# Performance work log

Measured on AMD Instinct MI355X. Metric: run time of the kernel, lower is better.

The kernel has to match this reference:

```python
import jax, jax.numpy as jnp
import numpy as np

EPS = 1e-5  # BatchNorm1d default eps


def gcn_conv(x, src, dst, w, b, n):
    # src/dst already include self-loops. Symmetric normalization D^-1/2 (A+I) D^-1/2.
    deg = jnp.zeros((n,), x.dtype).at[dst].add(1.0)
    dinv = jnp.where(deg > 0, jax.lax.rsqrt(jnp.maximum(deg, 1.0)), 0.0)
    norm = dinv[src] * dinv[dst]                      # [E+N]
    h = x @ w                                          # [B, N, H]
    msg = h[:, src, :] * norm[None, :, None]           # gather + scale  [B, E+N, H]
    agg = jnp.zeros_like(h).at[:, dst, :].add(msg)     # scatter-add
    return agg + b


def batch_norm(h, gamma, beta):
    # training-mode BN over the flattened (B*N) axis, biased variance (torch BN forward)
    mu = h.mean(axis=(0, 1))
    var = ((h - mu) ** 2).mean(axis=(0, 1))
    return (h - mu) * jax.lax.rsqrt(var + EPS) * gamma + beta


def reference(x, edge_index, W1, b1, W2, b2, gamma1, beta1, gamma2, beta2, Wc, bc):
    n = x.shape[1]
    loops = jnp.arange(n)
    src = jnp.concatenate([edge_index[0], loops])
    dst = jnp.concatenate([edge_index[1], loops])
    h = jax.nn.relu(gcn_conv(x, src, dst, W1, b1, n))
    h = batch_norm(h, gamma1, beta1)
    # dropout(p=0.2) treated as identity (eval / deterministic reference)
    h = jax.nn.relu(gcn_conv(h, src, dst, W2, b2, n))
    h = batch_norm(h, gamma2, beta2)
    out = (h @ Wc + bc).squeeze(-1)                    # [B, N]
    return out


def setup_inputs() -> dict:
    key = jax.random.key(0)
    ks = jax.random.split(key, 8)
    B, N, E, F, H = 4, 20000, 320000, 64, 128
    s = lambda fan: 1.0 / np.sqrt(fan)
    return {
        "x": jax.random.normal(ks[0], (B, N, F), dtype=jnp.float32),
        "edge_index": jax.random.randint(ks[1], (2, E), 0, N, dtype=jnp.int64),
        "W1": jax.random.normal(ks[2], (F, H), dtype=jnp.float32) * s(F),
        "b1": jnp.zeros((H,), jnp.float32),
        "W2": jax.random.normal(ks[3], (H, H), dtype=jnp.float32) * s(H),
        "b2": jnp.zeros((H,), jnp.float32),
        "gamma1": jnp.ones((H,), jnp.float32),
        "beta1": jnp.zeros((H,), jnp.float32),
        "gamma2": jnp.ones((H,), jnp.float32),
        "beta2": jnp.zeros((H,), jnp.float32),
        "Wc": jax.random.normal(ks[4], (H, 1), dtype=jnp.float32) * s(H),
        "bc": jnp.zeros((1,), jnp.float32),
    }
```

## Files before the change

kernel.cpp:

```cpp
#include <hip/hip_runtime.h>

constexpr int Bb = 4;
constexpr int Nn = 20000;
constexpr int Ff = 64;
constexpr int Hh = 128;
constexpr float BN_EPS = 1e-5f;
constexpr int NSLOTS = 64;

typedef __attribute__((ext_vector_type(8))) short bf16x8;
typedef __attribute__((ext_vector_type(4))) float f32x4;

__device__ inline unsigned f2bf(float f) {
    unsigned u = __float_as_uint(f);
    return (u + 0x7fffu + ((u >> 16) & 1u)) >> 16;
}
__device__ inline unsigned pack2(float lo, float hi) { return f2bf(lo) | (f2bf(hi) << 16); }
__device__ inline float bf_lo(unsigned w) { return __uint_as_float(w << 16); }
__device__ inline float bf_hi(unsigned w) { return __uint_as_float(w & 0xffff0000u); }

template <int NU>
__device__ inline void ldrow(unsigned* u, const unsigned* p) {
    if constexpr (NU == 2) { const uint2 t = *(const uint2*)p; u[0] = t.x; u[1] = t.y; }
    else { const uint4 t = *(const uint4*)p; u[0] = t.x; u[1] = t.y; u[2] = t.z; u[3] = t.w; }
}
template <int NU>
__device__ inline void acc_row(float* a, const unsigned* u, float nm) {
#pragma unroll
    for (int c = 0; c < NU; ++c) {
        a[2 * c]     = fmaf(nm, bf_lo(u[c]), a[2 * c]);
        a[2 * c + 1] = fmaf(nm, bf_hi(u[c]), a[2 * c + 1]);
    }
}

__global__ __launch_bounds__(256) void k_pre(const int* __restrict__ dst, int E,
                                             int NDEG,
                                             int* __restrict__ deg,
                                             const float* __restrict__ x,
                                             unsigned* __restrict__ xb,
                                             const float* __restrict__ W1,
                                             unsigned short* __restrict__ WTf) {
    const int b = blockIdx.x;
    if (b < NDEG) {
        const int e = b * 256 + threadIdx.x;
        if (e < E) atomicAdd(&deg[dst[e]], 1);
    } else if (b < NDEG + (Bb * Nn * 32) / 256) {
        const int t = (b - NDEG) * 256 + threadIdx.x;
        const int c2 = t & 31;
        const int bn = t >> 5;
        const int n  = bn % Nn;
        const int bb = bn / Nn;
        const float2 v = *(const float2*)&x[(size_t)t * 2];
        xb[((size_t)n * Bb + bb) * 32 + c2] = pack2(v.x, v.y);
    } else {
        const int f = (b - NDEG - (Bb * Nn * 32) / 256) * 256 + threadIdx.x;
        if (f < 128 * Ff) {
            const int j = f & 7, lane = (f >> 3) & 63, rest = f >> 9;
            const int ks = rest & 1, tt = rest >> 1;
            const int col = tt * 16 + (lane & 15);
            const int k = ks * 32 + ((lane >> 4) << 3) + j;
            WTf[f] = (unsigned short)f2bf(W1[(size_t)k * 128 + col]);
        }
    }
}

__global__ __launch_bounds__(1024) void k_scan(const int* __restrict__ deg,
                                               int* __restrict__ rowptr,
                                               int* __restrict__ cursor,
                                               float* __restrict__ dinv) {
    __shared__ int wsum[16];
    __shared__ int carry_s, tsum_s;
    const int tid = threadIdx.x;
    const int lane = tid & 63, wid = tid >> 6;
    if (tid == 0) carry_s = 0;
    __syncthreads();
    for (int base = 0; base < Nn; base += 1024) {
        const int i = base + tid;
        const int cnt = (i < Nn) ? (deg[i] + 1) : 0;
        int v = cnt;
#pragma unroll
        for (int d = 1; d < 64; d <<= 1) {
            const int t = __shfl_up(v, d);
            if (lane >= d) v += t;
        }
        if (lane == 63) wsum[wid] = v;
        __syncthreads();
        if (wid == 0) {
            const int orig = (lane < 16) ? wsum[lane] : 0;
            int w = orig;
#pragma unroll
            for (int d = 1; d < 16; d <<= 1) {
                const int t = __shfl_up(w, d);
                if (lane >= d) w += t;
            }
            if (lane == 15) tsum_s = w;
            if (lane < 16) wsum[lane] = w - orig;
        }
        __syncthreads();
        const int c = carry_s;
        const int excl = c + wsum[wid] + (v - cnt);
        if (i < Nn) {
            rowptr[i] = excl;
            cursor[i] = excl;
            dinv[i]   = rsqrtf((float)cnt);
        }
        __syncthreads();
        if (tid == 0) carry_s += tsum_s;
    }
    if (tid == 0) rowptr[Nn] = carry_s;
}

__global__ void k_fill(const int* __restrict__ src, const int* __restrict__ dst, int E,
                       const float* __restrict__ dinv, int* __restrict__ cursor,
                       int* __restrict__ csr_src, float* __restrict__ csr_norm,
                       float* __restrict__ nsum) {
    int t = blockIdx.x * blockDim.x + threadIdx.x;
    int s, d;
    if (t < E) { s = src[t]; d = dst[t]; }
    else if (t < E + Nn) { s = d = t - E; }
    else return;
    int pos = atomicAdd(&cursor[d], 1);
    const float nm = dinv[s] * dinv[d];
    csr_src[pos]  = s;
    csr_norm[pos] = nm;
    atomicAdd(&nsum[d], nm);
}

__global__ __launch_bounds__(256) void k_stat(const unsigned* __restrict__ h,
                                              float* __restrict__ gsum,
                                              float* __restrict__ gsq) {
    __shared__ float lsum[128], lsq[128];
    const int tid = threadIdx.x;
    if (tid < 128) { lsum[tid] = 0.f; lsq[tid] = 0.f; }
    __syncthreads();
    constexpr int TOTAL = Bb * Nn * (Hh / 2);
    const int stride = gridDim.x * 256;
    float s0 = 0.f, s1 = 0.f, q0 = 0.f, q1 = 0.f;
    for (int i = blockIdx.x * 256 + tid; i < TOTAL; i += stride) {
        const unsigned w = h[i];
        const float lo = bf_lo(w), hi = bf_hi(w);
        s0 += lo; s1 += hi;
        q0 = fmaf(lo, lo, q0); q1 = fmaf(hi, hi, q1);
    }
    const int c0 = (tid & 63) * 2;
    atomicAdd(&lsum[c0], s0);     atomicAdd(&lsum[c0 + 1], s1);
    atomicAdd(&lsq[c0],  q0);     atomicAdd(&lsq[c0 + 1],  q1);
    __syncthreads();
    float* gs = gsum + (size_t)(blockIdx.x & (NSLOTS - 1)) * 128;
    float* gq = gsq  + (size_t)(blockIdx.x & (NSLOTS - 1)) * 128;
    if (tid < 128) { atomicAdd(&gs[tid], lsum[tid]); atomicAdd(&gq[tid], lsq[tid]); }
}

__global__ __launch_bounds__(128) void k_prep2(const float* __restrict__ gsum,
                                               const float* __restrict__ gsq,
                                               const float* __restrict__ gamma,
                                               const float* __restrict__ beta,
                                               const float* __restrict__ W2,
                                               unsigned short* __restrict__ WT2f,
                                               float* __restrict__ shW2) {
    __shared__ float sc_s[128], sh_s[128];
    const int c = threadIdx.x;
    float s = 0.f, q = 0.f;
    for (int j = 0; j < NSLOTS; ++j) { s += gsum[j * 128 + c]; q += gsq[j * 128 + c]; }
    const float inv = 1.0f / (float)(Bb * Nn);
    const float mu  = s * inv;
    const float var = q * inv - mu * mu;
    const float sc  = gamma[c] * rsqrtf(var + BN_EPS);
    sc_s[c] = sc;
    sh_s[c] = beta[c] - mu * sc;
    __syncthreads();
    if (blockIdx.x < 64) {
#pragma unroll
        for (int i = 0; i < 2; ++i) {
            const int f = blockIdx.x * 256 + i * 128 + c;
            const int j = f & 7, lane = (f >> 3) & 63, rest = f >> 9;
            const int ks = rest & 3, tt = rest >> 2;
            const int col = tt * 16 + (lane & 15);
            const int k = ks * 32 + ((lane >> 4) << 3) + j;
            WT2f[f] = (unsigned short)f2bf(sc_s[k] * W2[(size_t)k * 128 + col]);
        }
    } else {
        float a = 0.f;
        for (int k = 0; k < 128; ++k) a = fmaf(sh_s[k], W2[(size_t)k * 128 + c], a);
        shW2[c] = a;
    }
}

template <int K, bool L2E>
__global__ __launch_bounds__(64, 8) void k_fmm(const unsigned* __restrict__ G,
                                               const int* __restrict__ rowptr,
                                               const int* __restrict__ csr_src,
                                               const float* __restrict__ csr_norm,
                                               const unsigned short* __restrict__ WTf,
                                               const float* __restrict__ bias,
                                               const float* __restrict__ nsum,
                                               const float* __restrict__ shW2,
                                               unsigned short* __restrict__ Yout) {
    constexpr int NKS = K / 32;
    constexpr int AST = K + 8;
    constexpr int NU = K / 32;
    constexpr int ROWU = Bb * K / 2;
    __shared__ alignas(16) unsigned short sA[16 * AST];
    __shared__ alignas(16) unsigned short sO[8 * 128];

    const int lane = threadIdx.x;
    const int cg = lane & 15, kg = lane >> 4;
    const int g = blockIdx.x;
    const int row0 = g * 8;

#pragma unroll
    for (int j = 0; j < 2; ++j) {
        const int v = g * 2 + j;
        const int beg = rowptr[v], end = rowptr[v + 1];
        float a[2 * NU];
#pragma unroll
        for (int c = 0; c < 2 * NU; ++c) a[c] = 0.f;
        int e = beg;
        for (; e + 8 <= end; e += 8) {
            unsigned u[8][NU];
            int si[8];
#pragma unroll
            for (int q = 0; q < 8; ++q) si[q] = csr_src[e + q];
#pragma unroll
            for (int q = 0; q < 8; ++q)
                ldrow<NU>(u[q], G + (size_t)si[q] * ROWU + lane * NU);
#pragma unroll
            for (int q = 0; q < 8; ++q) acc_row<NU>(a, u[q], csr_norm[e + q]);
        }
        for (; e + 4 <= end; e += 4) {
            unsigned u[4][NU];
            int si[4];
#pragma unroll
            for (int q = 0; q < 4; ++q) si[q] = csr_src[e + q];
#pragma unroll
            for (int q = 0; q < 4; ++q)
                ldrow<NU>(u[q], G + (size_t)si[q] * ROWU + lane * NU);
#pragma unroll
            for (int q = 0; q < 4; ++q) acc_row<NU>(a, u[q], csr_norm[e + q]);
        }
        for (; e < end; ++e) {
            unsigned u[NU];
            ldrow<NU>(u, G + (size_t)csr_src[e] * ROWU + lane * NU);
            acc_row<NU>(a, u, csr_norm[e]);
        }
        const int row = j * 4 + kg;
        unsigned p[NU];
#pragma unroll
        for (int c = 0; c < NU; ++c) p[c] = pack2(a[2 * c], a[2 * c + 1]);
        if constexpr (NU == 2) *(uint2*)&sA[row * AST + cg * 4] = *(const uint2*)p;
        else                   *(uint4*)&sA[row * AST + cg * 8] = *(const uint4*)p;
    }

    f32x4 acc[8];
#pragma unroll
    for (int t = 0; t < 8; ++t) acc[t] = (f32x4){0.f, 0.f, 0.f, 0.f};
#pragma unroll
    for (int ks = 0; ks < NKS; ++ks) {
        const bf16x8 av = *(const bf16x8*)&sA[cg * AST + ks * 32 + kg * 8];
#pragma unroll
        for (int t = 0; t < 8; ++t) {
            const bf16x8 bv = *(const bf16x8*)&WTf[(size_t)((t * NKS + ks) * 64 + lane) * 8];
            acc[t] = __builtin_amdgcn_mfma_f32_16x16x32_bf16(av, bv, acc[t], 0, 0, 0);
        }
    }

    if (kg < 2) {
        const int rbase = kg * 4;
        float ns = 0.f;
        if (L2E) ns = nsum[g * 2 + kg];
#pragma unroll
        for (int t = 0; t < 8; ++t) {
            const int col = t * 16 + cg;
            float badd = bias[col];
            if (L2E) badd = fmaf(ns, shW2[col], badd);
#pragma unroll
            for (int jj = 0; jj < 4; ++jj) {
                const float y = fmaxf(acc[t][jj] + badd, 0.f);
                sO[(rbase + jj) * 128 + col] = (unsigned short)f2bf(y);
            }
        }
    }
    const size_t obase = (size_t)row0 * 128;
#pragma unroll
    for (int h = 0; h < 2; ++h) {
        const int i16 = h * 64 + lane;
        *(uint4*)&Yout[obase + (size_t)i16 * 8] = *(const uint4*)&sO[i16 * 8];
    }
}

__global__ void k_bnfin2(const float* __restrict__ gsum, const float* __restrict__ gsq,
                         const float* __restrict__ gamma, const float* __restrict__ beta,
                         const float* __restrict__ Wc, const float* __restrict__ bc,
                         float* __restrict__ wcs, float* __restrict__ kc) {
    __shared__ float red[128];
    const int c = threadIdx.x;
    float s = 0.f, q = 0.f;
    for (int j = 0; j < NSLOTS; ++j) { s += gsum[j * 128 + c]; q += gsq[j * 128 + c]; }
    const float inv = 1.0f / (float)(Bb * Nn);
    const float mu  = s * inv;
    const float var = q * inv - mu * mu;
    const float sc  = gamma[c] * rsqrtf(var + BN_EPS);
    const float sh  = beta[c] - mu * sc;
    const float w   = Wc[c];
    wcs[c] = sc * w;
    red[c] = sh * w;
    __syncthreads();
    for (int st = 64; st; st >>= 1) {
        if (c < st) red[c] += red[c + st];
        __syncthreads();
    }
    if (c == 0) kc[0] = red[0] + bc[0];
}

__global__ __launch_bounds__(256) void k_cls(const unsigned* __restrict__ h2,
                                             const float* __restrict__ wcs,
                                             const float* __restrict__ kc,
                                             float* __restrict__ out) {
    const int wave = threadIdx.x >> 6;
    const int lane = threadIdx.x & 63;
    const size_t row = (size_t)blockIdx.x * 4 + wave;
    if (row >= (size_t)Bb * Nn) return;
    const unsigned w = h2[row * 64 + lane];
    const float2 wc = *(const float2*)&wcs[lane * 2];
    float p = bf_lo(w) * wc.x + bf_hi(w) * wc.y;
#pragma unroll
    for (int off = 32; off; off >>= 1) p += __shfl_down(p, off);
    if (lane == 0) {
        const int n = (int)(row >> 2), b = (int)(row & 3);
        out[(size_t)b * Nn + n] = p + kc[0];
    }
}

extern "C" void kernel_launch(void* const* d_in, const int* in_sizes, int n_in,
                              void* d_out, int out_size, void* d_ws, size_t ws_size,
                              hipStream_t stream) {
    const float* x      = (const float*)d_in[0];
    const int*   ei     = (const int*)d_in[1];
    const float* W1     = (const float*)d_in[2];
    const float* b1     = (const float*)d_in[3];
    const float* W2     = (const float*)d_in[4];
    const float* b2     = (const float*)d_in[5];
    const float* gamma1 = (const float*)d_in[6];
    const float* beta1  = (const float*)d_in[7];
    const float* gamma2 = (const float*)d_in[8];
    const float* beta2  = (const float*)d_in[9];
    const float* Wc     = (const float*)d_in[10];
    const float* bc     = (const float*)d_in[11];
    float* out = (float*)d_out;

    const int E = in_sizes[1] / 2;
    const int* src = ei;
    const int* dst = ei + E;

    char* ws = (char*)d_ws;
    size_t off = 0;
    auto alloc = [&](size_t bytes) -> char* {
        char* p = ws + off;
        off += (bytes + 255) & ~(size_t)255;
        return p;
    };
    int*      deg      = (int*)     alloc((size_t)Nn * 4);
    float*    nsum     = (float*)   alloc((size_t)Nn * 4);
    float*    gstat    = (float*)   alloc((size_t)4 * NSLOTS * 128 * 4);
    const size_t zspan = (size_t)((char*)(gstat + 4 * NSLOTS * 128) - (char*)deg);
    float* gsum1 = gstat;
    float* gsq1  = gstat + NSLOTS * 128;
    float* gsum2 = gstat + 2 * NSLOTS * 128;
    float* gsq2  = gstat + 3 * NSLOTS * 128;

    int*      cursor   = (int*)     alloc((size_t)Nn * 4);
    int*      rowptr   = (int*)     alloc((size_t)(Nn + 1) * 4);
    float*    dinv     = (float*)   alloc((size_t)Nn * 4);
    int*      csr_src  = (int*)     alloc((size_t)(E + Nn) * 4);
    float*    csr_norm = (float*)   alloc((size_t)(E + Nn) * 4);
    float*    wcs      = (float*)   alloc(128 * 4);
    float*    kc       = (float*)   alloc(256);
    unsigned short* WT1f = (unsigned short*)alloc((size_t)128 * Ff * 2);
    unsigned short* WT2f = (unsigned short*)alloc((size_t)128 * Hh * 2);
    float*          shW2 = (float*)         alloc((size_t)128 * 4);
    unsigned*       xb   = (unsigned*)      alloc((size_t)Nn * Bb * 32 * 4);
    unsigned short* h1b  = (unsigned short*)alloc((size_t)Bb * Nn * Hh * 2);
    unsigned short* h2b  = (unsigned short*)alloc((size_t)Bb * Nn * Hh * 2);

    (void)hipMemsetAsync(deg, 0, zspan, stream);

    const int NDEG = (E + 255) / 256;
    const int NCVT = (Bb * Nn * 32) / 256;
    k_pre<<<NDEG + NCVT + 32, 256, 0, stream>>>(dst, E, NDEG, deg, x, xb, W1, WT1f);
    k_scan<<<1, 1024, 0, stream>>>(deg, rowptr, cursor, dinv);
    k_fill<<<(E + Nn + 255) / 256, 256, 0, stream>>>(src, dst, E, dinv, cursor,
                                                     csr_src, csr_norm, nsum);

    k_fmm<Ff, false><<<Nn / 2, 64, 0, stream>>>(
        xb, rowptr, csr_src, csr_norm, WT1f, b1, nullptr, nullptr, h1b);
    k_stat<<<640, 256, 0, stream>>>((const unsigned*)h1b, gsum1, gsq1);
    k_prep2<<<65, 128, 0, stream>>>(gsum1, gsq1, gamma1, beta1, W2, WT2f, shW2);
    k_fmm<Hh, true><<<Nn / 2, 64, 0, stream>>>(
        (const unsigned*)h1b, rowptr, csr_src, csr_norm, WT2f, b2, nsum, shW2, h2b);
    k_stat<<<640, 256, 0, stream>>>((const unsigned*)h2b, gsum2, gsq2);
    k_bnfin2<<<1, Hh, 0, stream>>>(gsum2, gsq2, gamma2, beta2, Wc, bc, wcs, kc);

    k_cls<<<(Bb * Nn + 3) / 4, 256, 0, stream>>>((const unsigned*)h2b, wcs, kc, out);
}
```

Baseline: 215.6 us.

## Parallelize CSR scan, fuse BN finalize into stat kernel, trim fmm unroll and smem

Replaces the single-block serial prefix scan with a multi-block scan in which each block recomputes its prefix base by summing all earlier degrees. The second BN finalize is folded into the last-finishing k_stat block through an atomic counter and threadfence, which removes one kernel launch. The K=128 gather loop now unrolls by 4 instead of 8, and the output staging buffer for that variant aliases sA to cut shared memory use. These aim to reduce launch count, the serial scan latency and register/LDS pressure, at the cost of redundant prefix reads and last-block synchronization complexity.

```diff
diff --git a/kernel.cpp b/kernel.cpp
--- a/kernel.cpp
+++ b/kernel.cpp
@@ -6,6 +6,8 @@
 constexpr int Hh = 128;
 constexpr float BN_EPS = 1e-5f;
 constexpr int NSLOTS = 64;
+constexpr int NB = (Nn + 1023) / 1024;
+constexpr int NSTAT = 640;
 
 typedef __attribute__((ext_vector_type(8))) short bf16x8;
 typedef __attribute__((ext_vector_type(4))) float f32x4;
@@ -63,50 +65,57 @@
     }
 }
 
-__global__ __launch_bounds__(1024) void k_scan(const int* __restrict__ deg,
-                                               int* __restrict__ rowptr,
-                                               int* __restrict__ cursor,
-                                               float* __restrict__ dinv) {
-    __shared__ int wsum[16];
-    __shared__ int carry_s, tsum_s;
-    const int tid = threadIdx.x;
-    const int lane = tid & 63, wid = tid >> 6;
-    if (tid == 0) carry_s = 0;
-    __syncthreads();
-    for (int base = 0; base < Nn; base += 1024) {
-        const int i = base + tid;
-        const int cnt = (i < Nn) ? (deg[i] + 1) : 0;
-        int v = cnt;
-#pragma unroll
-        for (int d = 1; d < 64; d <<= 1) {
-            const int t = __shfl_up(v, d);
-            if (lane >= d) v += t;
-        }
-        if (lane == 63) wsum[wid] = v;
-        __syncthreads();
-        if (wid == 0) {
-            const int orig = (lane < 16) ? wsum[lane] : 0;
-            int w = orig;
-#pragma unroll
-            for (int d = 1; d < 16; d <<= 1) {
-                const int t = __shfl_up(w, d);
-                if (lane >= d) w += t;
-            }
-            if (lane == 15) tsum_s = w;
-            if (lane < 16) wsum[lane] = w - orig;
-        }
-        __syncthreads();
-        const int c = carry_s;
-        const int excl = c + wsum[wid] + (v - cnt);
-        if (i < Nn) {
-            rowptr[i] = excl;
-            cursor[i] = excl;
-            dinv[i]   = rsqrtf((float)cnt);
-        }
-        __syncthreads();
-        if (tid == 0) carry_s += tsum_s;
-    }
-    if (tid == 0) rowptr[Nn] = carry_s;
+__global__ __launch_bounds__(1024) void k_scanall(const int* __restrict__ deg,
+                                                  int* __restrict__ rowptr,
+                                                  int* __restrict__ cursor,
+                                                  float* __restrict__ dinv) {
+    __shared__ int red[16];
+    __shared__ int woff[16];
+    __shared__ int base_s;
+    const int tid = threadIdx.x, lane = tid & 63, wid = tid >> 6;
+    const int b = blockIdx.x;
+
+    int pre = 0;
+    for (int i = tid; i < b * 1024; i += 1024) pre += deg[i] + 1;
+#pragma unroll
+    for (int d = 32; d; d >>= 1) pre += __shfl_down(pre, d);
+    if (lane == 0) red[wid] = pre;
+    __syncthreads();
+    if (tid == 0) {
+        int s = 0;
+        for (int w = 0; w < 16; ++w) s += red[w];
+        base_s = s;
+    }
+
+    const int i = b * 1024 + tid;
+    const int cnt = (i < Nn) ? deg[i] + 1 : 0;
+    int v = cnt;
+#pragma unroll
+    for (int d = 1; d < 64; d <<= 1) {
+        const int t = __shfl_up(v, d);
+        if (lane >= d) v += t;
+    }
+    __syncthreads();
+    if (lane == 63) red[wid] = v;
+    __syncthreads();
+    if (wid == 0) {
+        const int orig = (lane < 16) ? red[lane] : 0;
+        int w = orig;
+#pragma unroll
+        for (int d = 1; d < 16; d <<= 1) {
+            const int t = __shfl_up(w, d);
+            if (lane >= d) w += t;
+        }
+        if (lane < 16) woff[lane] = w - orig;
+    }
+    __syncthreads();
+    if (i < Nn) {
+        const int excl = base_s + woff[wid] + (v - cnt);
+        rowptr[i] = excl;
+        cursor[i] = excl;
+        dinv[i] = rsqrtf((float)cnt);
+        if (i == Nn - 1) rowptr[Nn] = excl + cnt;
+    }
 }
 
 __global__ void k_fill(const int* __restrict__ src, const int* __restrict__ dst, int E,
@@ -125,9 +134,17 @@
     atomicAdd(&nsum[d], nm);
 }
 
+template <bool DO_FIN>
 __global__ __launch_bounds__(256) void k_stat(const unsigned* __restrict__ h,
                                               float* __restrict__ gsum,
-                                              float* __restrict__ gsq) {
+                                              float* __restrict__ gsq,
+                                              unsigned* __restrict__ cnt,
+                                              const float* __restrict__ gamma,
+                                              const float* __restrict__ beta,
+                                              const float* __restrict__ Wc,
+                                              const float* __restrict__ bc,
+                                              float* __restrict__ wcs,
+                                              float* __restrict__ kc) {
     __shared__ float lsum[128], lsq[128];
     const int tid = threadIdx.x;
     if (tid < 128) { lsum[tid] = 0.f; lsq[tid] = 0.f; }
@@ -148,6 +165,42 @@
     float* gs = gsum + (size_t)(blockIdx.x & (NSLOTS - 1)) * 128;
     float* gq = gsq  + (size_t)(blockIdx.x & (NSLOTS - 1)) * 128;
     if (tid < 128) { atomicAdd(&gs[tid], lsum[tid]); atomicAdd(&gq[tid], lsq[tid]); }
+
+    if constexpr (DO_FIN) {
+        __shared__ unsigned done_s;
+        __shared__ float red[128];
+        __threadfence();
+        __syncthreads();
+        if (tid == 0) done_s = atomicAdd(cnt, 1u);
+        __syncthreads();
+        if (done_s != gridDim.x - 1) return;
+        __threadfence();
+        if (tid < 128) {
+            const int c = tid;
+            float s = 0.f, q = 0.f;
+            for (int j = 0; j < NSLOTS; ++j) {
+                s += __hip_atomic_load(&gsum[j * 128 + c], __ATOMIC_RELAXED,
+                                       __HIP_MEMORY_SCOPE_AGENT);
+                q += __hip_atomic_load(&gsq[j * 128 + c], __ATOMIC_RELAXED,
+                                       __HIP_MEMORY_SCOPE_AGENT);
+            }
+            const float inv = 1.0f / (float)(Bb * Nn);
+            const float mu  = s * inv;
+            const float var = q * inv - mu * mu;
+            const float sc  = gamma[c] * rsqrtf(var + BN_EPS);
+            const float sh  = beta[c] - mu * sc;
+            const float w   = Wc[c];
+            wcs[c] = sc * w;
+            red[c] = sh * w;
+        }
+        __syncthreads();
+        if (tid < 64) {
+            float r = red[tid] + red[tid + 64];
+#pragma unroll
+            for (int off = 32; off; off >>= 1) r += __shfl_down(r, off);
+            if (tid == 0) kc[0] = r + bc[0];
+        }
+    }
 }
 
 __global__ __launch_bounds__(128) void k_prep2(const float* __restrict__ gsum,
@@ -198,9 +251,10 @@
     constexpr int NKS = K / 32;
     constexpr int AST = K + 8;
     constexpr int NU = K / 32;
+    constexpr int UNR = (K == 128) ? 4 : 8;
     constexpr int ROWU = Bb * K / 2;
-    __shared__ alignas(16) unsigned short sA[16 * AST];
-    __shared__ alignas(16) unsigned short sO[8 * 128];
+    __shared__ alignas(16) unsigned short sA[16 * AST + (K == 64 ? 1024 : 0)];
+    unsigned short* const sO = (K == 64) ? &sA[16 * AST] : &sA[8 * AST];
 
     const int lane = threadIdx.x;
     const int cg = lane & 15, kg = lane >> 4;
@@ -215,27 +269,16 @@
 #pragma unroll
         for (int c = 0; c < 2 * NU; ++c) a[c] = 0.f;
         int e = beg;
-        for (; e + 8 <= end; e += 8) {
-            unsigned u[8][NU];
-            int si[8];
-#pragma unroll
-            for (int q = 0; q < 8; ++q) si[q] = csr_src[e + q];
-#pragma unroll
-            for (int q = 0; q < 8; ++q)
+        for (; e + UNR <= end; e += UNR) {
+            unsigned u[UNR][NU];
+            int si[UNR];
+#pragma unroll
+            for (int q = 0; q < UNR; ++q) si[q] = csr_src[e + q];
+#pragma unroll
+            for (int q = 0; q < UNR; ++q)
                 ldrow<NU>(u[q], G + (size_t)si[q] * ROWU + lane * NU);
 #pragma unroll
-            for (int q = 0; q < 8; ++q) acc_row<NU>(a, u[q], csr_norm[e + q]);
-        }
-        for (; e + 4 <= end; e += 4) {
-            unsigned u[4][NU];
-            int si[4];
-#pragma unroll
-            for (int q = 0; q < 4; ++q) si[q] = csr_src[e + q];
-#pragma unroll
-            for (int q = 0; q < 4; ++q)
-                ldrow<NU>(u[q], G + (size_t)si[q] * ROWU + lane * NU);
-#pragma unroll
-            for (int q = 0; q < 4; ++q) acc_row<NU>(a, u[q], csr_norm[e + q]);
+            for (int q = 0; q < UNR; ++q) acc_row<NU>(a, u[q], csr_norm[e + q]);
         }
         for (; e < end; ++e) {
             unsigned u[NU];
@@ -285,30 +328,6 @@
         const int i16 = h * 64 + lane;
         *(uint4*)&Yout[obase + (size_t)i16 * 8] = *(const uint4*)&sO[i16 * 8];
     }
-}
-
-__global__ void k_bnfin2(const float* __restrict__ gsum, const float* __restrict__ gsq,
-                         const float* __restrict__ gamma, const float* __restrict__ beta,
-                         const float* __restrict__ Wc, const float* __restrict__ bc,
-                         float* __restrict__ wcs, float* __restrict__ kc) {
-    __shared__ float red[128];
-    const int c = threadIdx.x;
-    float s = 0.f, q = 0.f;
-    for (int j = 0; j < NSLOTS; ++j) { s += gsum[j * 128 + c]; q += gsq[j * 128 + c]; }
-    const float inv = 1.0f / (float)(Bb * Nn);
-    const float mu  = s * inv;
-    const float var = q * inv - mu * mu;
-    const float sc  = gamma[c] * rsqrtf(var + BN_EPS);
-    const float sh  = beta[c] - mu * sc;
-    const float w   = Wc[c];
-    wcs[c] = sc * w;
-    red[c] = sh * w;
-    __syncthreads();
-    for (int st = 64; st; st >>= 1) {
-        if (c < st) red[c] += red[c + st];
-        __syncthreads();
-    }
-    if (c == 0) kc[0] = red[0] + bc[0];
 }
 
 __global__ __launch_bounds__(256) void k_cls(const unsigned* __restrict__ h2,
@@ -361,7 +380,8 @@
     int*      deg      = (int*)     alloc((size_t)Nn * 4);
     float*    nsum     = (float*)   alloc((size_t)Nn * 4);
     float*    gstat    = (float*)   alloc((size_t)4 * NSLOTS * 128 * 4);
-    const size_t zspan = (size_t)((char*)(gstat + 4 * NSLOTS * 128) - (char*)deg);
+    unsigned* cnt      = (unsigned*)alloc(256);
+    const size_t zspan = (size_t)((char*)cnt + 256 - (char*)deg);
     float* gsum1 = gstat;
     float* gsq1  = gstat + NSLOTS * 128;
     float* gsum2 = gstat + 2 * NSLOTS * 128;
@@ -386,18 +406,20 @@
     const int NDEG = (E + 255) / 256;
     const int NCVT = (Bb * Nn * 32) / 256;
     k_pre<<<NDEG + NCVT + 32, 256, 0, stream>>>(dst, E, NDEG, deg, x, xb, W1, WT1f);
-    k_scan<<<1, 1024, 0, stream>>>(deg, rowptr, cursor, dinv);
+    k_scanall<<<NB, 1024, 0, stream>>>(deg, rowptr, cursor, dinv);
     k_fill<<<(E + Nn + 255) / 256, 256, 0, stream>>>(src, dst, E, dinv, cursor,
                                                      csr_src, csr_norm, nsum);
 
     k_fmm<Ff, false><<<Nn / 2, 64, 0, stream>>>(
         xb, rowptr, csr_src, csr_norm, WT1f, b1, nullptr, nullptr, h1b);
-    k_stat<<<640, 256, 0, stream>>>((const unsigned*)h1b, gsum1, gsq1);
+    k_stat<false><<<NSTAT, 256, 0, stream>>>((const unsigned*)h1b, gsum1, gsq1,
+                                             nullptr, nullptr, nullptr, nullptr,
+                                             nullptr, nullptr, nullptr);
     k_prep2<<<65, 128, 0, stream>>>(gsum1, gsq1, gamma1, beta1, W2, WT2f, shW2);
     k_fmm<Hh, true><<<Nn / 2, 64, 0, stream>>>(
         (const unsigned*)h1b, rowptr, csr_src, csr_norm, WT2f, b2, nsum, shW2, h2b);
-    k_stat<<<640, 256, 0, stream>>>((const unsigned*)h2b, gsum2, gsq2);
-    k_bnfin2<<<1, Hh, 0, stream>>>(gsum2, gsq2, gamma2, beta2, Wc, bc, wcs, kc);
+    k_stat<true><<<NSTAT, 256, 0, stream>>>((const unsigned*)h2b, gsum2, gsq2,
+                                            cnt, gamma2, beta2, Wc, bc, wcs, kc);
 
     k_cls<<<(Bb * Nn + 3) / 4, 256, 0, stream>>>((const unsigned*)h2b, wcs, kc, out);
 }
```

Result: slower. 234.0 us (+8.6%).
